# Kernel tuning notes

Hardware: AMD Instinct MI355X
Metric: run time of the kernel (lower is better)

The kernel has to match this reference:

```python
import jax, jax.numpy as jnp
import numpy as np

HEADS = 32
HEAD_DIM = 128
BLOCK = 64
THETA = 10000.0
MAXQ = 1024  # max q_seqlen in this batch (static)


def _rope(x, pos):
    # x: [T, H, D], pos: [T]  (Llama-style rotate_half RoPE)
    d = x.shape[-1]
    inv = 1.0 / (THETA ** (jnp.arange(0, d, 2, dtype=jnp.float32) / d))
    f = pos.astype(jnp.float32)[:, None] * inv[None, :]          # [T, D/2]
    emb = jnp.concatenate([f, f], axis=-1)                        # [T, D]
    cos = jnp.cos(emb)[:, None, :]
    sin = jnp.sin(emb)[:, None, :]
    x1, x2 = jnp.split(x, 2, axis=-1)
    rot = jnp.concatenate([-x2, x1], axis=-1)
    return x * cos + rot * sin


def setup_inputs() -> dict:
    key = jax.random.key(0)
    ks = jax.random.split(key, 8)
    hidden = HEADS * HEAD_DIM
    q_lens = np.array([1024, 512, 1024, 512])
    hist = np.array([512, 512, 0, 1024])
    kv_lens = q_lens + hist                    # [1536,1024,1024,1536]
    B = 4
    T = int(q_lens.sum())                      # 3072
    MAXB = 24                                  # max_kv 1536 / block 64
    NBLK = B * MAXB                            # 96
    q_start = np.concatenate([[0], np.cumsum(q_lens)[:-1]])
    pos = np.concatenate([h + np.arange(l) for h, l in zip(hist, q_lens)])
    w = lambda k: jax.random.normal(k, (hidden, hidden), jnp.float32) * 0.02
    return {
        'hidden_states': jax.random.normal(ks[0], (T, hidden), jnp.float32),
        'position_ids_1d': jnp.asarray(pos, jnp.int32),
        'q_start_loc': jnp.asarray(q_start, jnp.int32),
        'q_seqlens': jnp.asarray(q_lens, jnp.int32),
        'kv_seqlens': jnp.asarray(kv_lens, jnp.int32),
        'block_offsets': jnp.asarray(np.arange(NBLK).reshape(B, MAXB), jnp.int32),
        'past_key': jax.random.normal(ks[1], (NBLK, BLOCK, HEADS, HEAD_DIM), jnp.float32) * 0.5,
        'past_value': jax.random.normal(ks[2], (NBLK, BLOCK, HEADS, HEAD_DIM), jnp.float32) * 0.5,
        'Wq': w(ks[3]), 'bq': jnp.zeros((hidden,), jnp.float32),
        'Wk': w(ks[4]), 'bk': jnp.zeros((hidden,), jnp.float32),
        'Wv': w(ks[5]), 'bv': jnp.zeros((hidden,), jnp.float32),
        'Wo': w(ks[6]), 'bo': jnp.zeros((hidden,), jnp.float32),
    }


def reference(hidden_states, position_ids_1d, q_start_loc, q_seqlens, kv_seqlens,
              block_offsets, past_key, past_value,
              Wq, bq, Wk, bk, Wv, bv, Wo, bo):
    T, hidden = hidden_states.shape
    B, maxb = block_offsets.shape
    maxkv = maxb * BLOCK

    # fused QKV projections (nn.Linear: x @ W.T + b)
    q = (hidden_states @ Wq.T + bq).reshape(T, HEADS, HEAD_DIM)
    k = (hidden_states @ Wk.T + bk).reshape(T, HEADS, HEAD_DIM)
    v = (hidden_states @ Wv.T + bv).reshape(T, HEADS, HEAD_DIM)

    # rotary embedding on packed tokens
    q = _rope(q, position_ids_1d)
    k = _rope(k, position_ids_1d)

    # fill_kv_cache: scatter new k/v into paged cache after each seq's history
    tok = jnp.arange(T)
    seq_of = jnp.searchsorted(q_start_loc, tok, side='right') - 1   # [T]
    kvpos = kv_seqlens[seq_of] - q_seqlens[seq_of] + (tok - q_start_loc[seq_of])
    blk = block_offsets[seq_of, kvpos // BLOCK]
    off = kvpos % BLOCK
    kcache = past_key.at[blk, off].set(k)
    vcache = past_value.at[blk, off].set(v)

    # paged attention: gather per-seq K/V pages -> padded [B, maxkv, H, D]
    kf = kcache[block_offsets].reshape(B, maxkv, HEADS, HEAD_DIM)
    vf = vcache[block_offsets].reshape(B, maxkv, HEADS, HEAD_DIM)

    # pad packed queries -> [B, MAXQ, H, D]
    qi = jnp.arange(MAXQ)
    tok_idx = q_start_loc[:, None] + qi[None, :]
    validq = qi[None, :] < q_seqlens[:, None]                       # [B, MAXQ]
    tokc = jnp.clip(tok_idx, 0, T - 1)
    qp = q[tokc]                                                     # [B, MAXQ, H, D]

    scale = 1.0 / jnp.sqrt(jnp.float32(HEAD_DIM))
    scores = jnp.einsum('bqhd,bkhd->bhqk', qp, kf) * scale           # [B,H,MAXQ,maxkv]
    kj = jnp.arange(maxkv)
    # causal over history: key pos j allowed iff j <= hist[b] + i
    allow = kj[None, None, :] <= ((kv_seqlens - q_seqlens)[:, None, None] + qi[None, :, None])
    scores = jnp.where(allow[:, None, :, :], scores, -1e9)
    probs = jax.nn.softmax(scores, axis=-1)
    o = jnp.einsum('bhqk,bkhd->bqhd', probs, vf)                     # [B,MAXQ,H,D]
    o = o * validq[:, :, None, None]

    # unpad back to packed layout (invalid rows contribute zeros)
    packed = jnp.zeros((T, HEADS, HEAD_DIM), o.dtype).at[tokc.reshape(-1)].add(
        o.reshape(-1, HEADS, HEAD_DIM))
    out = packed.reshape(T, hidden) @ Wo.T + bo
    return out
```

## Files before the change

kernel.cpp:

```cpp
#include <hip/hip_runtime.h>
#include <hip/hip_bf16.h>

typedef unsigned short u16;
typedef __bf16 bf16x8 __attribute__((ext_vector_type(8)));
typedef float f32x4 __attribute__((ext_vector_type(4)));

#define N_HEADS 32
#define HD 128
#define HIDDEN 4096

__device__ __forceinline__ u16 f2bf(float x) {
    union { float f; unsigned u; } v; v.f = x;
    unsigned r = v.u + 0x7fffu + ((v.u >> 16) & 1u);
    return (u16)(r >> 16);
}
__device__ __forceinline__ float bf2f(u16 x) {
    return __uint_as_float((unsigned)x << 16);
}
__device__ __forceinline__ void gload_lds16(const void* g, void* l) {
    __builtin_amdgcn_global_load_lds(
        (const __attribute__((address_space(1))) unsigned*)g,
        (__attribute__((address_space(3))) unsigned*)l, 16, 0, 0);
}

__global__ __launch_bounds__(256) void cast_kernel(
    const float* __restrict__ Wq, const float* __restrict__ Wk,
    const float* __restrict__ Wv, const float* __restrict__ Wo,
    const float* __restrict__ H,
    const float* __restrict__ bq, const float* __restrict__ bk,
    const float* __restrict__ bv,
    u16* __restrict__ wsW, u16* __restrict__ wsWo, u16* __restrict__ wsH,
    float* __restrict__ wsB, long hsz)
{
    const long WSZ = (long)HIDDEN * HIDDEN;
    long total4 = (WSZ * 4 + hsz) >> 2;
    for (long i = (long)blockIdx.x * blockDim.x + threadIdx.x; i < total4;
         i += (long)gridDim.x * blockDim.x) {
        long e = i << 2;
        const float* src; u16* dst;
        if (e < WSZ)            { src = Wq + e;           dst = wsW + e; }
        else if (e < 2*WSZ)     { src = Wk + (e - WSZ);   dst = wsW + e; }
        else if (e < 3*WSZ)     { src = Wv + (e - 2*WSZ); dst = wsW + e; }
        else if (e < 4*WSZ)     { src = Wo + (e - 3*WSZ); dst = wsWo + (e - 3*WSZ); }
        else                    { src = H  + (e - 4*WSZ); dst = wsH  + (e - 4*WSZ); }
        float4 v = *(const float4*)src;
        ushort4 o; o.x = f2bf(v.x); o.y = f2bf(v.y); o.z = f2bf(v.z); o.w = f2bf(v.w);
        *(ushort4*)dst = o;
    }
    for (int i = blockIdx.x * blockDim.x + threadIdx.x; i < 3 * HIDDEN;
         i += gridDim.x * blockDim.x) {
        wsB[i] = (i < HIDDEN) ? bq[i] : (i < 2*HIDDEN ? bk[i - HIDDEN] : bv[i - 2*HIDDEN]);
    }
}

__global__ __launch_bounds__(256) void gemm_bt(
    const u16* __restrict__ A, const u16* __restrict__ Bt,
    const float* __restrict__ bias, void* __restrict__ Cout,
    int M, int N, int K, int out_bf16)
{
    __shared__ u16 As[128 * 32];
    __shared__ u16 Bs[128 * 32];
    const int tid = threadIdx.x;
    const int w = tid >> 6, lane = tid & 63;
    const int qd = lane >> 4, l15 = lane & 15;
    const int bm = blockIdx.x, bn = blockIdx.y;
    const int wm = w >> 1, wn = w & 1;
    f32x4 acc[4][4] = {};
    const int srow = lane >> 2;
    const int scol = (lane & 3) * 8;
    const long Ar = (long)bm * 128 + w * 32 + srow;
    const long Br = (long)bn * 128 + w * 32 + srow;
    for (int k0 = 0; k0 < K; k0 += 32) {
        __syncthreads();
        gload_lds16(A  + Ar * K        + k0 + scol, (char*)As + (w*32     ) * 64);
        gload_lds16(A  + (Ar + 16) * K + k0 + scol, (char*)As + (w*32 + 16) * 64);
        gload_lds16(Bt + Br * K        + k0 + scol, (char*)Bs + (w*32     ) * 64);
        gload_lds16(Bt + (Br + 16) * K + k0 + scol, (char*)Bs + (w*32 + 16) * 64);
        __syncthreads();
        bf16x8 a[4], b[4];
#pragma unroll
        for (int mt = 0; mt < 4; mt++)
            a[mt] = *(const bf16x8*)&As[(wm*64 + mt*16 + l15) * 32 + qd * 8];
#pragma unroll
        for (int nt = 0; nt < 4; nt++)
            b[nt] = *(const bf16x8*)&Bs[(wn*64 + nt*16 + l15) * 32 + qd * 8];
#pragma unroll
        for (int mt = 0; mt < 4; mt++)
#pragma unroll
            for (int nt = 0; nt < 4; nt++)
                acc[mt][nt] = __builtin_amdgcn_mfma_f32_16x16x32_bf16(
                    a[mt], b[nt], acc[mt][nt], 0, 0, 0);
    }
#pragma unroll
    for (int nt = 0; nt < 4; nt++) {
        int n = bn*128 + wn*64 + nt*16 + l15;
        float bv = bias[n];
#pragma unroll
        for (int mt = 0; mt < 4; mt++) {
            int m0 = bm*128 + wm*64 + mt*16 + qd*4;
#pragma unroll
            for (int r = 0; r < 4; r++) {
                float v = acc[mt][nt][r] + bv;
                if (out_bf16) ((u16*)Cout)[(long)(m0 + r) * N + n] = f2bf(v);
                else          ((float*)Cout)[(long)(m0 + r) * N + n] = v;
            }
        }
    }
}

__global__ __launch_bounds__(256) void rope_scatter(
    const u16* __restrict__ qkv, const int* __restrict__ pos_ids,
    const int* __restrict__ q_start, const int* __restrict__ q_lens,
    const int* __restrict__ kv_lens, const int* __restrict__ blk_off,
    float* __restrict__ pk, float* __restrict__ pv, u16* __restrict__ qr,
    int Bn, int maxb)
{
    int t = blockIdx.x >> 3;
    int h = ((blockIdx.x & 7) << 2) + (threadIdx.x >> 6);
    int d = threadIdx.x & 63;
    int b = 0;
    for (int i = 1; i < Bn; i++) if (t >= q_start[i]) b = i;
    int pos = pos_ids[t];
    float inv = exp2f(-(float)d * (13.287712379549449f / 64.0f));
    float f = (float)pos * inv;
    float cs = cosf(f), sn = sinf(f);
    const u16* row = qkv + (long)t * (3 * HIDDEN);
    float q1 = bf2f(row[h*HD + d]);
    float q2 = bf2f(row[h*HD + d + 64]);
    long qbase = ((long)t * N_HEADS + h) * HD + d;
    qr[qbase]      = f2bf(q1 * cs - q2 * sn);
    qr[qbase + 64] = f2bf(q2 * cs + q1 * sn);
    float k1 = bf2f(row[HIDDEN + h*HD + d]);
    float k2 = bf2f(row[HIDDEN + h*HD + d + 64]);
    float v1 = bf2f(row[2*HIDDEN + h*HD + d]);
    float v2 = bf2f(row[2*HIDDEN + h*HD + d + 64]);
    int kvpos = kv_lens[b] - q_lens[b] + (t - q_start[b]);
    int blk = blk_off[b * maxb + (kvpos >> 6)];
    int off = kvpos & 63;
    long base = (((long)blk * 64 + off) * N_HEADS + h) * HD + d;
    pk[base]      = k1 * cs - k2 * sn;
    pk[base + 64] = k2 * cs + k1 * sn;
    pv[base]      = v1;
    pv[base + 64] = v2;
}

__global__ __launch_bounds__(256) void attn_kernel(
    const u16* __restrict__ Qr, const float* __restrict__ pk,
    const float* __restrict__ pv,
    const int* __restrict__ q_start, const int* __restrict__ q_lens,
    const int* __restrict__ kv_lens, const int* __restrict__ blk_off,
    u16* __restrict__ aout, int Bn, int maxb, int ntiles)
{
    __shared__ u16 Qs[4 * 64 * 32];
    __shared__ u16 Ks[4 * 64 * 32];
    __shared__ u16 Vt[2 * 128 * 32];
    __shared__ u16 Ps[4 * 2 * 16 * 32];
    int tile = blockIdx.x % ntiles;
    int h    = blockIdx.x / ntiles;
    int b = 0, q0 = 0, acc = 0;
    for (int i = 0; i < Bn; i++) {
        int nt = q_lens[i] >> 6;
        if (tile >= acc && tile < acc + nt) { b = i; q0 = (tile - acc) << 6; }
        acc += nt;
    }
    int hist = kv_lens[b] - q_lens[b];
    int tok0 = q_start[b] + q0;
    int nchunk = ((hist + q0) >> 6) + 1;
    const int tid = threadIdx.x, w = tid >> 6, lane = tid & 63;
    const int qd = lane >> 4, l15 = lane & 15;

    for (int i = 0; i < 8; i++) {
        int idx = i * 1024 + tid * 4;
        int row = idx >> 7, d = idx & 127;
        const u16* src = Qr + ((long)(tok0 + row) * N_HEADS + h) * HD + d;
        uint2 v = *(const uint2*)src;
        *(uint2*)&Qs[(d >> 5) * 2048 + row * 32 + (d & 31)] = v;
    }
    float mstate[4], lstate[4];
    f32x4 o[8];
#pragma unroll
    for (int r = 0; r < 4; r++) { mstate[r] = -1e30f; lstate[r] = 0.f; }
#pragma unroll
    for (int dt = 0; dt < 8; dt++) o[dt] = (f32x4){0.f, 0.f, 0.f, 0.f};
    const float scale = 0.08838834764831845f;

    for (int c = 0; c < nchunk; c++) {
        int blk = blk_off[b * maxb + c];
        const float* kb = pk + ((long)blk * 64 * N_HEADS + h) * HD;
        const float* vb = pv + ((long)blk * 64 * N_HEADS + h) * HD;
        __syncthreads();
        for (int i = 0; i < 8; i++) {
            int idx = i * 1024 + tid * 4;
            int key = idx >> 7, d = idx & 127;
            float4 k4 = *(const float4*)(kb + (long)key * (N_HEADS * HD) + d);
            ushort4 o4; o4.x = f2bf(k4.x); o4.y = f2bf(k4.y);
            o4.z = f2bf(k4.z); o4.w = f2bf(k4.w);
            *(ushort4*)&Ks[(d >> 5) * 2048 + key * 32 + (d & 31)] = o4;
        }
        {
            int key = tid >> 2;
            int ks2 = key >> 5, k32 = key & 31;
            for (int i = 0; i < 8; i++) {
                int d = ((tid & 3) << 2) + (i << 4);
                float4 v4 = *(const float4*)(vb + (long)key * (N_HEADS * HD) + d);
                Vt[ks2 * 4096 + (d + 0) * 32 + k32] = f2bf(v4.x);
                Vt[ks2 * 4096 + (d + 1) * 32 + k32] = f2bf(v4.y);
                Vt[ks2 * 4096 + (d + 2) * 32 + k32] = f2bf(v4.z);
                Vt[ks2 * 4096 + (d + 3) * 32 + k32] = f2bf(v4.w);
            }
        }
        __syncthreads();
        f32x4 s[4] = {};
#pragma unroll
        for (int ks = 0; ks < 4; ks++) {
            bf16x8 aq = *(const bf16x8*)&Qs[ks * 2048 + (w * 16 + l15) * 32 + qd * 8];
#pragma unroll
            for (int nt = 0; nt < 4; nt++) {
                bf16x8 bk = *(const bf16x8*)&Ks[ks * 2048 + (nt * 16 + l15) * 32 + qd * 8];
                s[nt] = __builtin_amdgcn_mfma_f32_16x16x32_bf16(aq, bk, s[nt], 0, 0, 0);
            }
        }
        int rowbase = q0 + w * 16 + qd * 4;
        int keybase = c * 64;
        bool needmask = (keybase + 63) > (hist + q0 + w * 16);
        float p[4][4];
#pragma unroll
        for (int r = 0; r < 4; r++) {
            float vmax = -1e30f;
#pragma unroll
            for (int nt = 0; nt < 4; nt++) {
                float sv = s[nt][r] * scale;
                if (needmask && (keybase + nt * 16 + l15) > (hist + rowbase + r))
                    sv = -1e30f;
                p[nt][r] = sv;
                vmax = fmaxf(vmax, sv);
            }
            for (int off = 1; off < 16; off <<= 1)
                vmax = fmaxf(vmax, __shfl_xor(vmax, off, 64));
            float mn = fmaxf(mstate[r], vmax);
            float al = __expf(mstate[r] - mn);
            mstate[r] = mn;
            float rs = 0.f;
#pragma unroll
            for (int nt = 0; nt < 4; nt++) {
                float pe = __expf(p[nt][r] - mn);
                p[nt][r] = pe; rs += pe;
            }
            for (int off = 1; off < 16; off <<= 1)
                rs += __shfl_xor(rs, off, 64);
            lstate[r] = lstate[r] * al + rs;
#pragma unroll
            for (int dt = 0; dt < 8; dt++) o[dt][r] *= al;
        }
#pragma unroll
        for (int nt = 0; nt < 4; nt++) {
            int n = nt * 16 + l15;
#pragma unroll
            for (int r = 0; r < 4; r++)
                Ps[w * 1024 + (n >> 5) * 512 + (qd * 4 + r) * 32 + (n & 31)] = f2bf(p[nt][r]);
        }
#pragma unroll
        for (int ks2 = 0; ks2 < 2; ks2++) {
            bf16x8 ap = *(const bf16x8*)&Ps[w * 1024 + ks2 * 512 + l15 * 32 + qd * 8];
#pragma unroll
            for (int dt = 0; dt < 8; dt++) {
                bf16x8 bv = *(const bf16x8*)&Vt[ks2 * 4096 + (dt * 16 + l15) * 32 + qd * 8];
                o[dt] = __builtin_amdgcn_mfma_f32_16x16x32_bf16(ap, bv, o[dt], 0, 0, 0);
            }
        }
    }
#pragma unroll
    for (int dt = 0; dt < 8; dt++) {
        int d = dt * 16 + l15;
#pragma unroll
        for (int r = 0; r < 4; r++) {
            int token = tok0 + w * 16 + qd * 4 + r;
            aout[((long)token * N_HEADS + h) * HD + d] = f2bf(o[dt][r] / lstate[r]);
        }
    }
}

extern "C" void kernel_launch(void* const* d_in, const int* in_sizes, int n_in,
                              void* d_out, int out_size, void* d_ws, size_t ws_size,
                              hipStream_t stream)
{
    const float* H   = (const float*)d_in[0];
    const int* pos   = (const int*)d_in[1];
    const int* qst   = (const int*)d_in[2];
    const int* qln   = (const int*)d_in[3];
    const int* kvln  = (const int*)d_in[4];
    const int* boff  = (const int*)d_in[5];
    float* pk        = (float*)d_in[6];
    float* pv        = (float*)d_in[7];
    const float* Wq  = (const float*)d_in[8];
    const float* bq  = (const float*)d_in[9];
    const float* Wk  = (const float*)d_in[10];
    const float* bk  = (const float*)d_in[11];
    const float* Wv  = (const float*)d_in[12];
    const float* bv  = (const float*)d_in[13];
    const float* Wo  = (const float*)d_in[14];
    const float* bo  = (const float*)d_in[15];
    float* out = (float*)d_out;

    int T    = in_sizes[0] / HIDDEN;
    int Bn   = in_sizes[2];
    int maxb = in_sizes[5] / Bn;

    char* p = (char*)d_ws;
    u16* wsW   = (u16*)p;  p += (long)3 * HIDDEN * HIDDEN * 2;
    u16* wsWo  = (u16*)p;  p += (long)HIDDEN * HIDDEN * 2;
    u16* wsH   = (u16*)p;  p += (long)T * HIDDEN * 2;
    u16* wsQKV = (u16*)p;  p += (long)T * 3 * HIDDEN * 2;
    u16* wsQr  = (u16*)p;  p += (long)T * HIDDEN * 2;
    u16* wsAO  = (u16*)p;  p += (long)T * HIDDEN * 2;
    float* wsB = (float*)p;

    cast_kernel<<<2048, 256, 0, stream>>>(Wq, Wk, Wv, Wo, H, bq, bk, bv,
                                          wsW, wsWo, wsH, wsB, (long)T * HIDDEN);
    dim3 g1(T / 128, (3 * HIDDEN) / 128);
    gemm_bt<<<g1, 256, 0, stream>>>(wsH, wsW, wsB, wsQKV, T, 3 * HIDDEN, HIDDEN, 1);
    rope_scatter<<<T * 8, 256, 0, stream>>>(wsQKV, pos, qst, qln, kvln, boff,
                                            pk, pv, wsQr, Bn, maxb);
    int ntiles = T / 64;
    attn_kernel<<<ntiles * N_HEADS, 256, 0, stream>>>(wsQr, pk, pv, qst, qln, kvln,
                                                      boff, wsAO, Bn, maxb, ntiles);
    dim3 g2(T / 128, HIDDEN / 128);
    gemm_bt<<<g2, 256, 0, stream>>>(wsAO, wsWo, bo, out, T, HIDDEN, HIDDEN, 0);
}
```

Baseline: 1.496 ms.

## Pre-pack KV cache to bf16 tiles and streamline attention softmax

Result: faster. 1.224 ms (-18.2%).

```diff
diff --git a/kernel.cpp b/kernel.cpp
--- a/kernel.cpp
+++ b/kernel.cpp
@@ -3,6 +3,7 @@
 
 typedef unsigned short u16;
 typedef __bf16 bf16x8 __attribute__((ext_vector_type(8)));
+typedef short s16x4 __attribute__((ext_vector_type(4)));
 typedef float f32x4 __attribute__((ext_vector_type(4)));
 
 #define N_HEADS 32
@@ -16,6 +17,11 @@
 }
 __device__ __forceinline__ float bf2f(u16 x) {
     return __uint_as_float((unsigned)x << 16);
+}
+__device__ __forceinline__ unsigned pack_bf16(float a, float b) {
+    unsigned ua = __float_as_uint(a) + 0x8000u;
+    unsigned ub = __float_as_uint(b) + 0x8000u;
+    return __builtin_amdgcn_perm(ub, ua, 0x07060302);
 }
 __device__ __forceinline__ void gload_lds16(const void* g, void* l) {
     __builtin_amdgcn_global_load_lds(
@@ -108,54 +114,92 @@
     }
 }
 
-__global__ __launch_bounds__(256) void rope_scatter(
-    const u16* __restrict__ qkv, const int* __restrict__ pos_ids,
-    const int* __restrict__ q_start, const int* __restrict__ q_lens,
-    const int* __restrict__ kv_lens, const int* __restrict__ blk_off,
-    float* __restrict__ pk, float* __restrict__ pv, u16* __restrict__ qr,
-    int Bn, int maxb)
+__global__ __launch_bounds__(256) void rope_inplace(
+    u16* __restrict__ qkv, const int* __restrict__ pos_ids)
 {
     int t = blockIdx.x >> 3;
     int h = ((blockIdx.x & 7) << 2) + (threadIdx.x >> 6);
     int d = threadIdx.x & 63;
-    int b = 0;
-    for (int i = 1; i < Bn; i++) if (t >= q_start[i]) b = i;
     int pos = pos_ids[t];
     float inv = exp2f(-(float)d * (13.287712379549449f / 64.0f));
     float f = (float)pos * inv;
     float cs = cosf(f), sn = sinf(f);
-    const u16* row = qkv + (long)t * (3 * HIDDEN);
+    const float qscale = 0.08838834764831845f;
+    u16* row = qkv + (long)t * (3 * HIDDEN);
     float q1 = bf2f(row[h*HD + d]);
     float q2 = bf2f(row[h*HD + d + 64]);
-    long qbase = ((long)t * N_HEADS + h) * HD + d;
-    qr[qbase]      = f2bf(q1 * cs - q2 * sn);
-    qr[qbase + 64] = f2bf(q2 * cs + q1 * sn);
+    row[h*HD + d]      = f2bf((q1 * cs - q2 * sn) * qscale);
+    row[h*HD + d + 64] = f2bf((q2 * cs + q1 * sn) * qscale);
     float k1 = bf2f(row[HIDDEN + h*HD + d]);
     float k2 = bf2f(row[HIDDEN + h*HD + d + 64]);
-    float v1 = bf2f(row[2*HIDDEN + h*HD + d]);
-    float v2 = bf2f(row[2*HIDDEN + h*HD + d + 64]);
-    int kvpos = kv_lens[b] - q_lens[b] + (t - q_start[b]);
-    int blk = blk_off[b * maxb + (kvpos >> 6)];
-    int off = kvpos & 63;
-    long base = (((long)blk * 64 + off) * N_HEADS + h) * HD + d;
-    pk[base]      = k1 * cs - k2 * sn;
-    pk[base + 64] = k2 * cs + k1 * sn;
-    pv[base]      = v1;
-    pv[base + 64] = v2;
-}
-
-__global__ __launch_bounds__(256) void attn_kernel(
-    const u16* __restrict__ Qr, const float* __restrict__ pk,
-    const float* __restrict__ pv,
+    row[HIDDEN + h*HD + d]      = f2bf(k1 * cs - k2 * sn);
+    row[HIDDEN + h*HD + d + 64] = f2bf(k2 * cs + k1 * sn);
+}
+
+__global__ __launch_bounds__(256) void kvtransform(
+    const float* __restrict__ pk, const float* __restrict__ pv,
+    const u16* __restrict__ qkv,
+    const int* __restrict__ q_start, const int* __restrict__ q_lens,
+    const int* __restrict__ kv_lens, const int* __restrict__ blk_off,
+    u16* __restrict__ Kc, u16* __restrict__ Vc, int maxb)
+{
+    int b = blockIdx.x / maxb, c = blockIdx.x % maxb;
+    int h = blockIdx.y;
+    int kvlen = kv_lens[b];
+    if (c * 64 >= kvlen) return;
+    int hist = kvlen - q_lens[b];
+    int t0 = q_start[b];
+    int blk = blk_off[b * maxb + c];
+    const int tid = threadIdx.x;
+    u16* kout = Kc + ((long)blk * N_HEADS + h) * 8192;
+    u16* vout = Vc + ((long)blk * N_HEADS + h) * 9216;
+#pragma unroll
+    for (int r = 0; r < 8; r++) {
+        int i = r * 256 + tid;
+        int quad = i & 7, key = (i >> 3) & 63, ks = i >> 9;
+        int kvpos = c * 64 + key;
+        ushort4 o4;
+        if (kvpos < hist) {
+            float4 f = *(const float4*)(pk + (((long)blk*64 + key)*N_HEADS + h)*HD
+                                           + ks*32 + quad*4);
+            o4.x = f2bf(f.x); o4.y = f2bf(f.y); o4.z = f2bf(f.z); o4.w = f2bf(f.w);
+        } else {
+            int tok = t0 + kvpos - hist;
+            o4 = *(const ushort4*)(qkv + (long)tok*(3*HIDDEN) + HIDDEN
+                                      + h*HD + ks*32 + quad*4);
+        }
+        *(ushort4*)(kout + (long)i * 4) = o4;
+    }
+#pragma unroll
+    for (int r = 0; r < 8; r++) {
+        int i = r * 256 + tid;
+        int kq = i & 15, d = i >> 4;
+        ushort4 o4; u16* o = (u16*)&o4;
+#pragma unroll
+        for (int j = 0; j < 4; j++) {
+            int key = kq * 4 + j;
+            int kvpos = c * 64 + key;
+            if (kvpos < hist)
+                o[j] = f2bf(pv[(((long)blk*64 + key)*N_HEADS + h)*HD + d]);
+            else {
+                int tok = t0 + kvpos - hist;
+                o[j] = qkv[(long)tok*(3*HIDDEN) + 2*HIDDEN + h*HD + d];
+            }
+        }
+        *(ushort4*)(vout + (long)d * 72 + kq * 4) = o4;
+    }
+}
+
+__global__ __launch_bounds__(256, 4) void attn_kernel(
+    const u16* __restrict__ qkv, const u16* __restrict__ Kc,
+    const u16* __restrict__ Vc,
     const int* __restrict__ q_start, const int* __restrict__ q_lens,
     const int* __restrict__ kv_lens, const int* __restrict__ blk_off,
     u16* __restrict__ aout, int Bn, int maxb, int ntiles)
 {
-    __shared__ u16 Qs[4 * 64 * 32];
     __shared__ u16 Ks[4 * 64 * 32];
-    __shared__ u16 Vt[2 * 128 * 32];
-    __shared__ u16 Ps[4 * 2 * 16 * 32];
-    int tile = blockIdx.x % ntiles;
+    __shared__ u16 Vt[128 * 72];
+    int tile = ntiles - 1 - (blockIdx.x % ntiles);
     int h    = blockIdx.x / ntiles;
     int b = 0, q0 = 0, acc = 0;
     for (int i = 0; i < Bn; i++) {
@@ -165,117 +209,86 @@
     }
     int hist = kv_lens[b] - q_lens[b];
     int tok0 = q_start[b] + q0;
-    int nchunk = ((hist + q0) >> 6) + 1;
+    int nchunk = (hist + q0 + 63) / 64 + 1;
     const int tid = threadIdx.x, w = tid >> 6, lane = tid & 63;
     const int qd = lane >> 4, l15 = lane & 15;
 
-    for (int i = 0; i < 8; i++) {
-        int idx = i * 1024 + tid * 4;
-        int row = idx >> 7, d = idx & 127;
-        const u16* src = Qr + ((long)(tok0 + row) * N_HEADS + h) * HD + d;
-        uint2 v = *(const uint2*)src;
-        *(uint2*)&Qs[(d >> 5) * 2048 + row * 32 + (d & 31)] = v;
-    }
-    float mstate[4], lstate[4];
-    f32x4 o[8];
-#pragma unroll
-    for (int r = 0; r < 4; r++) { mstate[r] = -1e30f; lstate[r] = 0.f; }
-#pragma unroll
-    for (int dt = 0; dt < 8; dt++) o[dt] = (f32x4){0.f, 0.f, 0.f, 0.f};
-    const float scale = 0.08838834764831845f;
+    const u16* qrow = qkv + (long)(tok0 + w*16 + l15) * (3*HIDDEN) + h * HD;
+    bf16x8 qf[4];
+#pragma unroll
+    for (int ds = 0; ds < 4; ds++)
+        qf[ds] = *(const bf16x8*)(qrow + ds*32 + qd*8);
+
+    f32x4 o[8] = {};
+    f32x4 lsum = {};
+    const s16x4 ONES = { (short)0x3F80, (short)0x3F80, (short)0x3F80, (short)0x3F80 };
+    const int qglob = hist + q0 + w*16 + l15;
 
     for (int c = 0; c < nchunk; c++) {
         int blk = blk_off[b * maxb + c];
-        const float* kb = pk + ((long)blk * 64 * N_HEADS + h) * HD;
-        const float* vb = pv + ((long)blk * 64 * N_HEADS + h) * HD;
+        const u16* kg_ = Kc + ((long)blk * N_HEADS + h) * 8192;
+        const u16* vg_ = Vc + ((long)blk * N_HEADS + h) * 9216;
         __syncthreads();
-        for (int i = 0; i < 8; i++) {
-            int idx = i * 1024 + tid * 4;
-            int key = idx >> 7, d = idx & 127;
-            float4 k4 = *(const float4*)(kb + (long)key * (N_HEADS * HD) + d);
-            ushort4 o4; o4.x = f2bf(k4.x); o4.y = f2bf(k4.y);
-            o4.z = f2bf(k4.z); o4.w = f2bf(k4.w);
-            *(ushort4*)&Ks[(d >> 5) * 2048 + key * 32 + (d & 31)] = o4;
-        }
-        {
-            int key = tid >> 2;
-            int ks2 = key >> 5, k32 = key & 31;
-            for (int i = 0; i < 8; i++) {
-                int d = ((tid & 3) << 2) + (i << 4);
-                float4 v4 = *(const float4*)(vb + (long)key * (N_HEADS * HD) + d);
-                Vt[ks2 * 4096 + (d + 0) * 32 + k32] = f2bf(v4.x);
-                Vt[ks2 * 4096 + (d + 1) * 32 + k32] = f2bf(v4.y);
-                Vt[ks2 * 4096 + (d + 2) * 32 + k32] = f2bf(v4.z);
-                Vt[ks2 * 4096 + (d + 3) * 32 + k32] = f2bf(v4.w);
-            }
+#pragma unroll
+        for (int r = 0; r < 4; r++) {
+            int idx = r*256 + w*64 + lane;
+            gload_lds16(kg_ + idx*8, Ks + idx*8);
+        }
+#pragma unroll
+        for (int r = 0; r < 4; r++) {
+            int idx = r*256 + w*64 + lane;
+            gload_lds16(vg_ + idx*8, Vt + idx*8);
+        }
+        if (w < 2) {
+            int idx = 1024 + w*64 + lane;
+            gload_lds16(vg_ + idx*8, Vt + idx*8);
         }
         __syncthreads();
         f32x4 s[4] = {};
 #pragma unroll
-        for (int ks = 0; ks < 4; ks++) {
-            bf16x8 aq = *(const bf16x8*)&Qs[ks * 2048 + (w * 16 + l15) * 32 + qd * 8];
-#pragma unroll
-            for (int nt = 0; nt < 4; nt++) {
-                bf16x8 bk = *(const bf16x8*)&Ks[ks * 2048 + (nt * 16 + l15) * 32 + qd * 8];
-                s[nt] = __builtin_amdgcn_mfma_f32_16x16x32_bf16(aq, bk, s[nt], 0, 0, 0);
-            }
-        }
-        int rowbase = q0 + w * 16 + qd * 4;
-        int keybase = c * 64;
-        bool needmask = (keybase + 63) > (hist + q0 + w * 16);
-        float p[4][4];
+        for (int ds = 0; ds < 4; ds++)
+#pragma unroll
+            for (int kg = 0; kg < 4; kg++) {
+                bf16x8 a = *(const bf16x8*)&Ks[ds*2048 + (kg*16 + l15)*32 + qd*8];
+                s[kg] = __builtin_amdgcn_mfma_f32_16x16x32_bf16(a, qf[ds], s[kg], 0, 0, 0);
+            }
+        bool needmask = (c*64 + 63) > (hist + q0 + w*16);
+#pragma unroll
+        for (int kg = 0; kg < 4; kg++) {
+            int keyb = c*64 + kg*16 + qd*4;
+            float pe0, pe1, pe2, pe3;
+            if (needmask) {
+                int thr = qglob - keyb;
+                pe0 = __expf(0 <= thr ? s[kg][0] : -1e30f);
+                pe1 = __expf(1 <= thr ? s[kg][1] : -1e30f);
+                pe2 = __expf(2 <= thr ? s[kg][2] : -1e30f);
+                pe3 = __expf(3 <= thr ? s[kg][3] : -1e30f);
+            } else {
+                pe0 = __expf(s[kg][0]); pe1 = __expf(s[kg][1]);
+                pe2 = __expf(s[kg][2]); pe3 = __expf(s[kg][3]);
+            }
+            union { unsigned u[2]; s16x4 v; } pu;
+            pu.u[0] = pack_bf16(pe0, pe1);
+            pu.u[1] = pack_bf16(pe2, pe3);
+            s16x4 p4 = pu.v;
+            lsum = __builtin_amdgcn_mfma_f32_16x16x16bf16_1k(p4, ONES, lsum, 0, 0, 0);
+#pragma unroll
+            for (int dt = 0; dt < 8; dt++) {
+                s16x4 b4 = *(const s16x4*)&Vt[(dt*16 + l15)*72 + kg*16 + qd*4];
+                o[dt] = __builtin_amdgcn_mfma_f32_16x16x16bf16_1k(p4, b4, o[dt], 0, 0, 0);
+            }
+        }
+    }
+    float inv[4];
+#pragma unroll
+    for (int r = 0; r < 4; r++) inv[r] = 1.0f / lsum[r];
+#pragma unroll
+    for (int dt = 0; dt < 8; dt++) {
+        int d = dt*16 + l15;
 #pragma unroll
         for (int r = 0; r < 4; r++) {
-            float vmax = -1e30f;
-#pragma unroll
-            for (int nt = 0; nt < 4; nt++) {
-                float sv = s[nt][r] * scale;
-                if (needmask && (keybase + nt * 16 + l15) > (hist + rowbase + r))
-                    sv = -1e30f;
-                p[nt][r] = sv;
-                vmax = fmaxf(vmax, sv);
-            }
-            for (int off = 1; off < 16; off <<= 1)
-                vmax = fmaxf(vmax, __shfl_xor(vmax, off, 64));
-            float mn = fmaxf(mstate[r], vmax);
-            float al = __expf(mstate[r] - mn);
-            mstate[r] = mn;
-            float rs = 0.f;
-#pragma unroll
-            for (int nt = 0; nt < 4; nt++) {
-                float pe = __expf(p[nt][r] - mn);
-                p[nt][r] = pe; rs += pe;
-            }
-            for (int off = 1; off < 16; off <<= 1)
-                rs += __shfl_xor(rs, off, 64);
-            lstate[r] = lstate[r] * al + rs;
-#pragma unroll
-            for (int dt = 0; dt < 8; dt++) o[dt][r] *= al;
-        }
-#pragma unroll
-        for (int nt = 0; nt < 4; nt++) {
-            int n = nt * 16 + l15;
-#pragma unroll
-            for (int r = 0; r < 4; r++)
-                Ps[w * 1024 + (n >> 5) * 512 + (qd * 4 + r) * 32 + (n & 31)] = f2bf(p[nt][r]);
-        }
-#pragma unroll
-        for (int ks2 = 0; ks2 < 2; ks2++) {
-            bf16x8 ap = *(const bf16x8*)&Ps[w * 1024 + ks2 * 512 + l15 * 32 + qd * 8];
-#pragma unroll
-            for (int dt = 0; dt < 8; dt++) {
-                bf16x8 bv = *(const bf16x8*)&Vt[ks2 * 4096 + (dt * 16 + l15) * 32 + qd * 8];
-                o[dt] = __builtin_amdgcn_mfma_f32_16x16x32_bf16(ap, bv, o[dt], 0, 0, 0);
-            }
-        }
-    }
-#pragma unroll
-    for (int dt = 0; dt < 8; dt++) {
-        int d = dt * 16 + l15;
-#pragma unroll
-        for (int r = 0; r < 4; r++) {
-            int token = tok0 + w * 16 + qd * 4 + r;
-            aout[((long)token * N_HEADS + h) * HD + d] = f2bf(o[dt][r] / lstate[r]);
+            int token = tok0 + w*16 + qd*4 + r;
+            aout[((long)token * N_HEADS + h) * HD + d] = f2bf(o[dt][r] * inv[r]);
         }
     }
 }
@@ -290,8 +303,8 @@
     const int* qln   = (const int*)d_in[3];
     const int* kvln  = (const int*)d_in[4];
     const int* boff  = (const int*)d_in[5];
-    float* pk        = (float*)d_in[6];
-    float* pv        = (float*)d_in[7];
+    const float* pk  = (const float*)d_in[6];
+    const float* pv  = (const float*)d_in[7];
     const float* Wq  = (const float*)d_in[8];
     const float* bq  = (const float*)d_in[9];
     const float* Wk  = (const float*)d_in[10];
@@ -305,25 +318,29 @@
     int T    = in_sizes[0] / HIDDEN;
     int Bn   = in_sizes[2];
     int maxb = in_sizes[5] / Bn;
+    int NBLK = in_sizes[6] / (64 * N_HEADS * HD);
 
     char* p = (char*)d_ws;
     u16* wsW   = (u16*)p;  p += (long)3 * HIDDEN * HIDDEN * 2;
     u16* wsWo  = (u16*)p;  p += (long)HIDDEN * HIDDEN * 2;
     u16* wsH   = (u16*)p;  p += (long)T * HIDDEN * 2;
     u16* wsQKV = (u16*)p;  p += (long)T * 3 * HIDDEN * 2;
-    u16* wsQr  = (u16*)p;  p += (long)T * HIDDEN * 2;
     u16* wsAO  = (u16*)p;  p += (long)T * HIDDEN * 2;
+    u16* wsKc  = (u16*)p;  p += (long)NBLK * N_HEADS * 8192 * 2;
+    u16* wsVc  = (u16*)p;  p += (long)NBLK * N_HEADS * 9216 * 2;
     float* wsB = (float*)p;
 
     cast_kernel<<<2048, 256, 0, stream>>>(Wq, Wk, Wv, Wo, H, bq, bk, bv,
                                           wsW, wsWo, wsH, wsB, (long)T * HIDDEN);
     dim3 g1(T / 128, (3 * HIDDEN) / 128);
     gemm_bt<<<g1, 256, 0, stream>>>(wsH, wsW, wsB, wsQKV, T, 3 * HIDDEN, HIDDEN, 1);
-    rope_scatter<<<T * 8, 256, 0, stream>>>(wsQKV, pos, qst, qln, kvln, boff,
-                                            pk, pv, wsQr, Bn, maxb);
+    rope_inplace<<<T * 8, 256, 0, stream>>>(wsQKV, pos);
+    dim3 g2(Bn * maxb, N_HEADS);
+    kvtransform<<<g2, 256, 0, stream>>>(pk, pv, wsQKV, qst, qln, kvln, boff,
+                                        wsKc, wsVc, maxb);
     int ntiles = T / 64;
-    attn_kernel<<<ntiles * N_HEADS, 256, 0, stream>>>(wsQr, pk, pv, qst, qln, kvln,
-                                                      boff, wsAO, Bn, maxb, ntiles);
-    dim3 g2(T / 128, HIDDEN / 128);
-    gemm_bt<<<g2, 256, 0, stream>>>(wsAO, wsWo, bo, out, T, HIDDEN, HIDDEN, 0);
-}
+    attn_kernel<<<ntiles * N_HEADS, 256, 0, stream>>>(wsQKV, wsKc, wsVc, qst, qln,
+                                                      kvln, boff, wsAO, Bn, maxb, ntiles);
+    dim3 g3(T / 128, HIDDEN / 128);
+    gemm_bt<<<g3, 256, 0, stream>>>(wsAO, wsWo, bo, out, T, HIDDEN, HIDDEN, 0);
+}
```
